# Kernel tuning notes

Measured on AMD Instinct MI355X. Metric: run time of the kernel, lower is better.

Reference implementation:

```python
import jax, jax.numpy as jnp
import numpy as np

N_NODES = 100000
N_EDGES = 1600000
NIN = 128
NOUT = 128


def setup_inputs() -> dict:
    key = jax.random.key(0)
    k1, k2, k3, k4, k5 = jax.random.split(key, 5)
    x = jax.random.normal(k1, (N_NODES, NIN), dtype=jnp.float32)
    edge_index = jax.random.randint(k2, (2, N_EDGES), 0, N_NODES, dtype=jnp.int32)
    edge_attr = jax.random.uniform(k3, (N_EDGES,), dtype=jnp.float32)
    # GCNConv linear weight (glorot-ish scale) and bias
    W = jax.random.normal(k4, (NIN, NOUT), dtype=jnp.float32) / np.sqrt(NIN)
    b = jnp.zeros((NOUT,), dtype=jnp.float32)
    return {"x": x, "edge_index": edge_index, "edge_attr": edge_attr, "W": W, "b": b}


def reference(x, edge_index, edge_attr, W, b):
    # PyG GCNConv: out = D^{-1/2} (A + I) D^{-1/2} X W + b
    # edge_attr is accepted by the wrapper's forward but ignored.
    N = x.shape[0]
    src, dst = edge_index[0], edge_index[1]
    # add self-loops
    loops = jnp.arange(N, dtype=edge_index.dtype)
    src = jnp.concatenate([src, loops])
    dst = jnp.concatenate([dst, loops])
    # degree over destination nodes (unit edge weights + self loops)
    deg = jax.ops.segment_sum(jnp.ones_like(dst, dtype=x.dtype), dst, num_segments=N)
    dinv = jnp.where(deg > 0, jax.lax.rsqrt(deg), 0.0)
    norm = dinv[src] * dinv[dst]  # [E + N]
    h = x @ W  # [N, NOUT] — project before aggregation (PyG order)
    msgs = h[src] * norm[:, None]  # [E + N, NOUT] gathered messages
    out = jax.ops.segment_sum(msgs, dst, num_segments=N) + b
    return out
```

## Files before the change

kernel.cpp:

```cpp
#include <hip/hip_runtime.h>
#include <hip/hip_bf16.h>


#define NIN 128
#define NOUT 128
#define MAXD 64
#define WPITCH 68
#define NB_BUILD 2048

typedef __attribute__((ext_vector_type(8))) short short8;
typedef __attribute__((ext_vector_type(4))) float f32x4;
typedef __attribute__((ext_vector_type(4))) int   i32x4;
typedef __attribute__((ext_vector_type(4))) float f32x4v;

__device__ __forceinline__ float bf2f(unsigned short u) {
    unsigned v = ((unsigned)u) << 16;
    return __uint_as_float(v);
}
__device__ __forceinline__ unsigned short f2bf(float f) {
    unsigned u = __float_as_uint(f);
    unsigned r = 0x7FFFu + ((u >> 16) & 1u);
    return (unsigned short)((u + r) >> 16);
}

__global__ __launch_bounds__(256, 8) void k_build(const float* __restrict__ x,
                                                  const float* __restrict__ W,
                                                  const int* __restrict__ ei,
                                                  int* __restrict__ cnt,
                                                  int* __restrict__ adj,
                                                  unsigned short* __restrict__ h,
                                                  int E, int N, int gb) {
    __shared__ unsigned short Wt[128 * WPITCH];

    int grp  = blockIdx.x >> 5;
    int slot = blockIdx.x & 31;
    int ngrp = gridDim.x >> 5;

    if (slot >= 24) {
        int rid = grp * 8 + (slot - 24);
        int nscat = ngrp * 8;
        int chunkE = (((E + nscat - 1) / nscat) + 3) & ~3;
        int e0 = rid * chunkE, e1 = min(E, e0 + chunkE);
        for (int e = e0 + (int)threadIdx.x * 4; e < e1; e += 1024) {
            i32x4 s4 = *(const i32x4*)(ei + e);
            i32x4 d4 = *(const i32x4*)(ei + E + e);
            #pragma unroll
            for (int k = 0; k < 4; k++) {
                int d = d4[k];
                int pos = atomicAdd(&cnt[d], 1);
                if (pos < MAXD) adj[(size_t)d * MAXD + pos] = s4[k];
            }
        }
        return;
    }

    int wave = threadIdx.x >> 6, lane = threadIdx.x & 63;
    int c = lane & 15, quad = lane >> 4;

    for (int t = grp * 24 + slot; t < gb; t += ngrp * 24) {
        int node_base = t * 64 + wave * 16;
        bool active = node_base < N;
        const f32x4v* xrow = (const f32x4v*)(x + (size_t)(node_base + c) * NIN + quad * 8);

        f32x4 acc[8];
        #pragma unroll
        for (int nt = 0; nt < 8; nt++) acc[nt] = (f32x4)(0.0f);

        __syncthreads();
        for (int idx = threadIdx.x; idx < 64 * 128; idx += 256) {
            int kk = idx >> 7, n = idx & 127;
            Wt[n * WPITCH + kk] = f2bf(W[kk * 128 + n]);
        }
        __syncthreads();

        if (active) {
            short8 a0, a1;
            f32x4v f0 = __builtin_nontemporal_load(xrow + 0);
            f32x4v f1 = __builtin_nontemporal_load(xrow + 1);
            f32x4v g0 = __builtin_nontemporal_load(xrow + 8);
            f32x4v g1 = __builtin_nontemporal_load(xrow + 9);
            a0[0]=(short)f2bf(f0[0]); a0[1]=(short)f2bf(f0[1]); a0[2]=(short)f2bf(f0[2]); a0[3]=(short)f2bf(f0[3]);
            a0[4]=(short)f2bf(f1[0]); a0[5]=(short)f2bf(f1[1]); a0[6]=(short)f2bf(f1[2]); a0[7]=(short)f2bf(f1[3]);
            a1[0]=(short)f2bf(g0[0]); a1[1]=(short)f2bf(g0[1]); a1[2]=(short)f2bf(g0[2]); a1[3]=(short)f2bf(g0[3]);
            a1[4]=(short)f2bf(g1[0]); a1[5]=(short)f2bf(g1[1]); a1[6]=(short)f2bf(g1[2]); a1[7]=(short)f2bf(g1[3]);
            #pragma unroll
            for (int nt = 0; nt < 8; nt++) {
                const unsigned short* wp = &Wt[(nt * 16 + c) * WPITCH + quad * 8];
                short8 b0 = *(const short8*)(wp);
                short8 b1 = *(const short8*)(wp + 32);
                acc[nt] = __builtin_amdgcn_mfma_f32_16x16x32_bf16(a0, b0, acc[nt], 0, 0, 0);
                acc[nt] = __builtin_amdgcn_mfma_f32_16x16x32_bf16(a1, b1, acc[nt], 0, 0, 0);
            }
        }
        __syncthreads();
        for (int idx = threadIdx.x; idx < 64 * 128; idx += 256) {
            int kk = idx >> 7, n = idx & 127;
            Wt[n * WPITCH + kk] = f2bf(W[(kk + 64) * 128 + n]);
        }
        __syncthreads();

        if (active) {
            short8 a2, a3;
            f32x4v f0 = __builtin_nontemporal_load(xrow + 16);
            f32x4v f1 = __builtin_nontemporal_load(xrow + 17);
            f32x4v g0 = __builtin_nontemporal_load(xrow + 24);
            f32x4v g1 = __builtin_nontemporal_load(xrow + 25);
            a2[0]=(short)f2bf(f0[0]); a2[1]=(short)f2bf(f0[1]); a2[2]=(short)f2bf(f0[2]); a2[3]=(short)f2bf(f0[3]);
            a2[4]=(short)f2bf(f1[0]); a2[5]=(short)f2bf(f1[1]); a2[6]=(short)f2bf(f1[2]); a2[7]=(short)f2bf(f1[3]);
            a3[0]=(short)f2bf(g0[0]); a3[1]=(short)f2bf(g0[1]); a3[2]=(short)f2bf(g0[2]); a3[3]=(short)f2bf(g0[3]);
            a3[4]=(short)f2bf(g1[0]); a3[5]=(short)f2bf(g1[1]); a3[6]=(short)f2bf(g1[2]); a3[7]=(short)f2bf(g1[3]);
            #pragma unroll
            for (int nt = 0; nt < 8; nt++) {
                const unsigned short* wp = &Wt[(nt * 16 + c) * WPITCH + quad * 8];
                short8 b0 = *(const short8*)(wp);
                short8 b1 = *(const short8*)(wp + 32);
                acc[nt] = __builtin_amdgcn_mfma_f32_16x16x32_bf16(a2, b0, acc[nt], 0, 0, 0);
                acc[nt] = __builtin_amdgcn_mfma_f32_16x16x32_bf16(a3, b1, acc[nt], 0, 0, 0);
            }

            #pragma unroll
            for (int nt = 0; nt < 8; nt++) {
                #pragma unroll
                for (int r = 0; r < 4; r++) {
                    int node = node_base + quad * 4 + r;
                    h[(size_t)node * NOUT + nt * 16 + c] = f2bf(acc[nt][r]);
                }
            }
        }
    }
}

__global__ __launch_bounds__(256) void k_scale(unsigned short* __restrict__ h,
                                               const int* __restrict__ cnt, int N) {
    int idx = blockIdx.x * 256 + threadIdx.x;
    int total = N * (NOUT / 8);
    if (idx >= total) return;
    int node = idx >> 4;
    float dv = rsqrtf((float)(cnt[node] + 1));
    uint4* hq = (uint4*)h;
    uint4 v = hq[idx];
    unsigned r[4] = { v.x, v.y, v.z, v.w };
    #pragma unroll
    for (int w = 0; w < 4; w++) {
        float lo = bf2f((unsigned short)(r[w] & 0xFFFF)) * dv;
        float hi = bf2f((unsigned short)(r[w] >> 16)) * dv;
        r[w] = (unsigned)f2bf(lo) | ((unsigned)f2bf(hi) << 16);
    }
    v.x = r[0]; v.y = r[1]; v.z = r[2]; v.w = r[3];
    hq[idx] = v;
}

__global__ __launch_bounds__(256) void k_agg(const unsigned short* __restrict__ h,
                                             const int* __restrict__ cnt,
                                             const int* __restrict__ adj,
                                             const float* __restrict__ bias,
                                             float* __restrict__ out, int N) {
    int wave = threadIdx.x >> 6, lane = threadIdx.x & 63;
    int half = lane >> 5, sub = lane & 31;
    int node = blockIdx.x * 4 + wave;
    if (node >= N) return;

    int degc = cnt[node];
    float dn = rsqrtf((float)(degc + 1));
    int e0 = node * MAXD;
    int e1 = e0 + min(degc, MAXD);

    const uint2* hp = (const uint2*)h;
    float a0 = 0.f, a1 = 0.f, a2 = 0.f, a3 = 0.f;

    {
        int s = half ? ((e0 < e1) ? adj[e0] : node) : node;
        uint2 v = hp[(size_t)s * 32 + sub];
        if (!half || (e0 < e1)) {
            a0 += bf2f((unsigned short)(v.x & 0xFFFF));
            a1 += bf2f((unsigned short)(v.x >> 16));
            a2 += bf2f((unsigned short)(v.y & 0xFFFF));
            a3 += bf2f((unsigned short)(v.y >> 16));
        }
    }

    int e = e0 + 1;
    for (; e + 7 < e1; e += 8) {
        #pragma unroll
        for (int k = 0; k < 4; k++) {
            int s = adj[e + 2 * k + half];
            uint2 v = hp[(size_t)s * 32 + sub];
            a0 += bf2f((unsigned short)(v.x & 0xFFFF));
            a1 += bf2f((unsigned short)(v.x >> 16));
            a2 += bf2f((unsigned short)(v.y & 0xFFFF));
            a3 += bf2f((unsigned short)(v.y >> 16));
        }
    }
    for (; e + 1 < e1; e += 2) {
        int s = adj[e + half];
        uint2 v = hp[(size_t)s * 32 + sub];
        a0 += bf2f((unsigned short)(v.x & 0xFFFF));
        a1 += bf2f((unsigned short)(v.x >> 16));
        a2 += bf2f((unsigned short)(v.y & 0xFFFF));
        a3 += bf2f((unsigned short)(v.y >> 16));
    }
    if (e < e1) {
        int s = adj[e];
        uint2 v = hp[(size_t)s * 32 + sub];
        if (!half) {
            a0 += bf2f((unsigned short)(v.x & 0xFFFF));
            a1 += bf2f((unsigned short)(v.x >> 16));
            a2 += bf2f((unsigned short)(v.y & 0xFFFF));
            a3 += bf2f((unsigned short)(v.y >> 16));
        }
    }

    a0 += __shfl_xor(a0, 32);
    a1 += __shfl_xor(a1, 32);
    a2 += __shfl_xor(a2, 32);
    a3 += __shfl_xor(a3, 32);

    if (!half) {
        float4 b4 = ((const float4*)bias)[sub];
        f32x4 o;
        o[0] = a0 * dn + b4.x;
        o[1] = a1 * dn + b4.y;
        o[2] = a2 * dn + b4.z;
        o[3] = a3 * dn + b4.w;
        __builtin_nontemporal_store(o, (f32x4*)(out + (size_t)node * NOUT) + sub);
    }
}

static inline size_t align256(size_t v) { return (v + 255) & ~(size_t)255; }

extern "C" void kernel_launch(void* const* d_in, const int* in_sizes, int n_in,
                              void* d_out, int out_size, void* d_ws, size_t ws_size,
                              hipStream_t stream) {
    const float* x  = (const float*)d_in[0];
    const int*   ei = (const int*)d_in[1];
    const float* W  = (const float*)d_in[3];
    const float* b  = (const float*)d_in[4];
    float*       out = (float*)d_out;

    int N = in_sizes[0] / NIN;
    int E = in_sizes[1] / 2;
    int gb = (N + 63) / 64;

    char* ws = (char*)d_ws;
    size_t o = 0;
    int*   cnt = (int*)(ws + o);   o += align256((size_t)N * 4);
    int*   adj = (int*)(ws + o);   o += align256((size_t)N * MAXD * 4);
    unsigned short* h = (unsigned short*)(ws + o); o += align256((size_t)N * NOUT * 2);
    (void)ws_size; (void)n_in; (void)out_size;

    hipMemsetAsync(cnt, 0, (size_t)N * 4, stream);
    k_build<<<NB_BUILD, 256, 0, stream>>>(x, W, ei, cnt, adj, h, E, N, gb);
    k_scale<<<(N * (NOUT / 8) + 255) / 256, 256, 0, stream>>>(h, cnt, N);
    k_agg<<<(N + 3) / 4, 256, 0, stream>>>(h, cnt, adj, b, out, N);
}
```

Baseline: 296.5 us.

## Partition edge scatter by destination range and give each node a half-wave in aggregation

```diff
diff --git a/kernel.cpp b/kernel.cpp
--- a/kernel.cpp
+++ b/kernel.cpp
@@ -4,9 +4,10 @@
 
 #define NIN 128
 #define NOUT 128
+#define NPART 8
+#define G_GROUPS 98
 #define MAXD 64
 #define WPITCH 68
-#define NB_BUILD 2048
 
 typedef __attribute__((ext_vector_type(8))) short short8;
 typedef __attribute__((ext_vector_type(4))) float f32x4;
@@ -36,20 +37,39 @@
     int slot = blockIdx.x & 31;
     int ngrp = gridDim.x >> 5;
 
-    if (slot >= 24) {
-        int rid = grp * 8 + (slot - 24);
-        int nscat = ngrp * 8;
-        int chunkE = (((E + nscat - 1) / nscat) + 3) & ~3;
-        int e0 = rid * chunkE, e1 = min(E, e0 + chunkE);
-        for (int e = e0 + (int)threadIdx.x * 4; e < e1; e += 1024) {
+    if (slot >= 8) {
+        int q = slot - 8;
+        int p = q & 7;
+        int j = q >> 3;
+        int PS = (N + NPART - 1) / NPART;
+        int lo = p * PS, hi = min(N, lo + PS);
+        int nchunk = 3 * ngrp;
+        int chunkE = (((E + nchunk - 1) / nchunk) + 3) & ~3;
+        int c = grp * 3 + j;
+        int e0 = c * chunkE, e1 = min(E, e0 + chunkE);
+
+        auto proc = [&](i32x4 s4, i32x4 d4) {
+            #pragma unroll
+            for (int k = 0; k < 4; k++) {
+                int d = d4[k];
+                if (d >= lo && d < hi) {
+                    int pos = atomicAdd(&cnt[d], 1);
+                    if (pos < MAXD) adj[(size_t)d * MAXD + pos] = s4[k];
+                }
+            }
+        };
+
+        int e = e0 + (int)threadIdx.x * 4;
+        if (e < e1) {
             i32x4 s4 = *(const i32x4*)(ei + e);
             i32x4 d4 = *(const i32x4*)(ei + E + e);
-            #pragma unroll
-            for (int k = 0; k < 4; k++) {
-                int d = d4[k];
-                int pos = atomicAdd(&cnt[d], 1);
-                if (pos < MAXD) adj[(size_t)d * MAXD + pos] = s4[k];
-            }
+            for (int en = e + 1024; en < e1; en += 1024) {
+                i32x4 s4n = *(const i32x4*)(ei + en);
+                i32x4 d4n = *(const i32x4*)(ei + E + en);
+                proc(s4, d4);
+                s4 = s4n; d4 = d4n;
+            }
+            proc(s4, d4);
         }
         return;
     }
@@ -57,7 +77,7 @@
     int wave = threadIdx.x >> 6, lane = threadIdx.x & 63;
     int c = lane & 15, quad = lane >> 4;
 
-    for (int t = grp * 24 + slot; t < gb; t += ngrp * 24) {
+    for (int t = grp * 8 + slot; t < gb; t += ngrp * 8) {
         int node_base = t * 64 + wave * 16;
         bool active = node_base < N;
         const f32x4v* xrow = (const f32x4v*)(x + (size_t)(node_base + c) * NIN + quad * 8);
@@ -155,9 +175,8 @@
                                              const int* __restrict__ adj,
                                              const float* __restrict__ bias,
                                              float* __restrict__ out, int N) {
-    int wave = threadIdx.x >> 6, lane = threadIdx.x & 63;
-    int half = lane >> 5, sub = lane & 31;
-    int node = blockIdx.x * 4 + wave;
+    int sub = threadIdx.x & 31;
+    int node = blockIdx.x * 8 + (threadIdx.x >> 5);
     if (node >= N) return;
 
     int degc = cnt[node];
@@ -166,64 +185,76 @@
     int e1 = e0 + min(degc, MAXD);
 
     const uint2* hp = (const uint2*)h;
-    float a0 = 0.f, a1 = 0.f, a2 = 0.f, a3 = 0.f;
-
+
+    float a0, a1, a2, a3;
     {
-        int s = half ? ((e0 < e1) ? adj[e0] : node) : node;
-        uint2 v = hp[(size_t)s * 32 + sub];
-        if (!half || (e0 < e1)) {
-            a0 += bf2f((unsigned short)(v.x & 0xFFFF));
-            a1 += bf2f((unsigned short)(v.x >> 16));
-            a2 += bf2f((unsigned short)(v.y & 0xFFFF));
-            a3 += bf2f((unsigned short)(v.y >> 16));
-        }
-    }
-
-    int e = e0 + 1;
+        uint2 v = hp[(size_t)node * 32 + sub];
+        a0 = bf2f((unsigned short)(v.x & 0xFFFF));
+        a1 = bf2f((unsigned short)(v.x >> 16));
+        a2 = bf2f((unsigned short)(v.y & 0xFFFF));
+        a3 = bf2f((unsigned short)(v.y >> 16));
+    }
+
+    int e = e0;
     for (; e + 7 < e1; e += 8) {
-        #pragma unroll
-        for (int k = 0; k < 4; k++) {
-            int s = adj[e + 2 * k + half];
-            uint2 v = hp[(size_t)s * 32 + sub];
-            a0 += bf2f((unsigned short)(v.x & 0xFFFF));
-            a1 += bf2f((unsigned short)(v.x >> 16));
-            a2 += bf2f((unsigned short)(v.y & 0xFFFF));
-            a3 += bf2f((unsigned short)(v.y >> 16));
-        }
-    }
-    for (; e + 1 < e1; e += 2) {
-        int s = adj[e + half];
+        i32x4 sA = *(const i32x4*)(adj + e);
+        i32x4 sB = *(const i32x4*)(adj + e + 4);
+        uint2 v0 = hp[(size_t)sA[0] * 32 + sub];
+        uint2 v1 = hp[(size_t)sA[1] * 32 + sub];
+        uint2 v2 = hp[(size_t)sA[2] * 32 + sub];
+        uint2 v3 = hp[(size_t)sA[3] * 32 + sub];
+        uint2 v4 = hp[(size_t)sB[0] * 32 + sub];
+        uint2 v5 = hp[(size_t)sB[1] * 32 + sub];
+        uint2 v6 = hp[(size_t)sB[2] * 32 + sub];
+        uint2 v7 = hp[(size_t)sB[3] * 32 + sub];
+        a0 += bf2f((unsigned short)(v0.x & 0xFFFF)) + bf2f((unsigned short)(v1.x & 0xFFFF))
+            + bf2f((unsigned short)(v2.x & 0xFFFF)) + bf2f((unsigned short)(v3.x & 0xFFFF))
+            + bf2f((unsigned short)(v4.x & 0xFFFF)) + bf2f((unsigned short)(v5.x & 0xFFFF))
+            + bf2f((unsigned short)(v6.x & 0xFFFF)) + bf2f((unsigned short)(v7.x & 0xFFFF));
+        a1 += bf2f((unsigned short)(v0.x >> 16)) + bf2f((unsigned short)(v1.x >> 16))
+            + bf2f((unsigned short)(v2.x >> 16)) + bf2f((unsigned short)(v3.x >> 16))
+            + bf2f((unsigned short)(v4.x >> 16)) + bf2f((unsigned short)(v5.x >> 16))
+            + bf2f((unsigned short)(v6.x >> 16)) + bf2f((unsigned short)(v7.x >> 16));
+        a2 += bf2f((unsigned short)(v0.y & 0xFFFF)) + bf2f((unsigned short)(v1.y & 0xFFFF))
+            + bf2f((unsigned short)(v2.y & 0xFFFF)) + bf2f((unsigned short)(v3.y & 0xFFFF))
+            + bf2f((unsigned short)(v4.y & 0xFFFF)) + bf2f((unsigned short)(v5.y & 0xFFFF))
+            + bf2f((unsigned short)(v6.y & 0xFFFF)) + bf2f((unsigned short)(v7.y & 0xFFFF));
+        a3 += bf2f((unsigned short)(v0.y >> 16)) + bf2f((unsigned short)(v1.y >> 16))
+            + bf2f((unsigned short)(v2.y >> 16)) + bf2f((unsigned short)(v3.y >> 16))
+            + bf2f((unsigned short)(v4.y >> 16)) + bf2f((unsigned short)(v5.y >> 16))
+            + bf2f((unsigned short)(v6.y >> 16)) + bf2f((unsigned short)(v7.y >> 16));
+    }
+    for (; e + 3 < e1; e += 4) {
+        i32x4 sA = *(const i32x4*)(adj + e);
+        uint2 v0 = hp[(size_t)sA[0] * 32 + sub];
+        uint2 v1 = hp[(size_t)sA[1] * 32 + sub];
+        uint2 v2 = hp[(size_t)sA[2] * 32 + sub];
+        uint2 v3 = hp[(size_t)sA[3] * 32 + sub];
+        a0 += bf2f((unsigned short)(v0.x & 0xFFFF)) + bf2f((unsigned short)(v1.x & 0xFFFF))
+            + bf2f((unsigned short)(v2.x & 0xFFFF)) + bf2f((unsigned short)(v3.x & 0xFFFF));
+        a1 += bf2f((unsigned short)(v0.x >> 16)) + bf2f((unsigned short)(v1.x >> 16))
+            + bf2f((unsigned short)(v2.x >> 16)) + bf2f((unsigned short)(v3.x >> 16));
+        a2 += bf2f((unsigned short)(v0.y & 0xFFFF)) + bf2f((unsigned short)(v1.y & 0xFFFF))
+            + bf2f((unsigned short)(v2.y & 0xFFFF)) + bf2f((unsigned short)(v3.y & 0xFFFF));
+        a3 += bf2f((unsigned short)(v0.y >> 16)) + bf2f((unsigned short)(v1.y >> 16))
+            + bf2f((unsigned short)(v2.y >> 16)) + bf2f((unsigned short)(v3.y >> 16));
+    }
+    for (; e < e1; e++) {
+        int s = adj[e];
         uint2 v = hp[(size_t)s * 32 + sub];
         a0 += bf2f((unsigned short)(v.x & 0xFFFF));
         a1 += bf2f((unsigned short)(v.x >> 16));
         a2 += bf2f((unsigned short)(v.y & 0xFFFF));
         a3 += bf2f((unsigned short)(v.y >> 16));
     }
-    if (e < e1) {
-        int s = adj[e];
-        uint2 v = hp[(size_t)s * 32 + sub];
-        if (!half) {
-            a0 += bf2f((unsigned short)(v.x & 0xFFFF));
-            a1 += bf2f((unsigned short)(v.x >> 16));
-            a2 += bf2f((unsigned short)(v.y & 0xFFFF));
-            a3 += bf2f((unsigned short)(v.y >> 16));
-        }
-    }
-
-    a0 += __shfl_xor(a0, 32);
-    a1 += __shfl_xor(a1, 32);
-    a2 += __shfl_xor(a2, 32);
-    a3 += __shfl_xor(a3, 32);
-
-    if (!half) {
-        float4 b4 = ((const float4*)bias)[sub];
-        f32x4 o;
-        o[0] = a0 * dn + b4.x;
-        o[1] = a1 * dn + b4.y;
-        o[2] = a2 * dn + b4.z;
-        o[3] = a3 * dn + b4.w;
-        __builtin_nontemporal_store(o, (f32x4*)(out + (size_t)node * NOUT) + sub);
-    }
+
+    float4 b4 = ((const float4*)bias)[sub];
+    f32x4 o;
+    o[0] = a0 * dn + b4.x;
+    o[1] = a1 * dn + b4.y;
+    o[2] = a2 * dn + b4.z;
+    o[3] = a3 * dn + b4.w;
+    __builtin_nontemporal_store(o, (f32x4*)(out + (size_t)node * NOUT) + sub);
 }
 
 static inline size_t align256(size_t v) { return (v + 255) & ~(size_t)255; }
@@ -249,7 +280,7 @@
     (void)ws_size; (void)n_in; (void)out_size;
 
     hipMemsetAsync(cnt, 0, (size_t)N * 4, stream);
-    k_build<<<NB_BUILD, 256, 0, stream>>>(x, W, ei, cnt, adj, h, E, N, gb);
+    k_build<<<32 * G_GROUPS, 256, 0, stream>>>(x, W, ei, cnt, adj, h, E, N, gb);
     k_scale<<<(N * (NOUT / 8) + 255) / 256, 256, 0, stream>>>(h, cnt, N);
-    k_agg<<<(N + 3) / 4, 256, 0, stream>>>(h, cnt, adj, b, out, N);
-}
+    k_agg<<<(N + 7) / 8, 256, 0, stream>>>(h, cnt, adj, b, out, N);
+}
```

New measurement: 313.0 us. +5.6%, slower.
